# Performance work log

Hardware: AMD Instinct MI355X
Metric: run time of the kernel (lower is better)

Reference implementation:

```python
import jax, jax.numpy as jnp
import numpy as np

B, T, D, H = 512, 1024, 12, 100


def setup_inputs() -> dict:
    key = jax.random.key(0)
    ks = jax.random.split(key, 5)
    x = jax.random.normal(ks[0], (B, T, D), dtype=jnp.float32)
    Wx = jax.random.normal(ks[1], (D, 4 * H), dtype=jnp.float32) * (1.0 / np.sqrt(D))
    Wh = jax.random.normal(ks[2], (H, 4 * H), dtype=jnp.float32) * (1.0 / np.sqrt(H))
    b = jnp.zeros((4 * H,), dtype=jnp.float32)
    Wd = jax.random.normal(ks[3], (H, D), dtype=jnp.float32) * (1.0 / np.sqrt(H))
    bd = jnp.zeros((D,), dtype=jnp.float32)
    return {"x": x, "Wx": Wx, "Wh": Wh, "b": b, "Wd": Wd, "bd": bd}


def _lstm_seq(x, Wx, Wh, b):
    # Precompute input projection for all timesteps (vectorized GEMM).
    xg = jnp.einsum('btd,dh->bth', x, Wx) + b  # [B, T, 4H]
    xg = jnp.transpose(xg, (1, 0, 2))          # [T, B, 4H] for scan

    def step(carry, xg_t):
        h, c = carry
        z = xg_t + h @ Wh                      # [B, 4H]
        i, f, g, o = jnp.split(z, 4, axis=-1)  # Keras gate order: i, f, c, o
        i = jax.nn.sigmoid(i)
        f = jax.nn.sigmoid(f)
        g = jnp.tanh(g)
        o = jax.nn.sigmoid(o)
        c = f * c + i * g
        h = o * jnp.tanh(c)
        return (h, c), h

    h0 = jnp.zeros((x.shape[0], Wh.shape[0]), dtype=x.dtype)
    c0 = jnp.zeros_like(h0)
    _, hs = jax.lax.scan(step, (h0, c0), xg)   # hs: [T, B, H]
    return jnp.transpose(hs, (1, 0, 2))        # [B, T, H]


def reference(x, Wx, Wh, b, Wd, bd):
    hs = _lstm_seq(x, Wx, Wh, b)               # [B, T, H]
    return jnp.einsum('bth,hd->btd', hs, Wd) + bd  # [B, T, 12]
```

## Files before the change

kernel.cpp:

```cpp
#include <hip/hip_runtime.h>
#include <math.h>

#define T_LEN 1024
#define BATCH 512
#define DIN   12
#define HID   100
#define G4    400
#define MB    4
#define NBLK  (BATCH / MB)
#define AROW  160
#define NW    8
#define NTHR  (NW * 64)
#define CHUNK 64
#define UNROLL 8

typedef _Float16 half8   __attribute__((ext_vector_type(8)));
typedef _Float16 half4_t __attribute__((ext_vector_type(4)));
typedef float    f32x4   __attribute__((ext_vector_type(4)));

static __device__ __forceinline__ float fast_exp2(float v) {
#if __has_builtin(__builtin_amdgcn_exp2f)
    return __builtin_amdgcn_exp2f(v);
#else
    return exp2f(v);
#endif
}
static __device__ __forceinline__ float fast_rcp(float v) {
#if __has_builtin(__builtin_amdgcn_rcpf)
    return __builtin_amdgcn_rcpf(v);
#else
    return 1.0f / v;
#endif
}

static __device__ __forceinline__ void wg_barrier_lds() {
    __builtin_amdgcn_sched_barrier(0);
    asm volatile("s_waitcnt lgkmcnt(0)" ::: "memory");
    __builtin_amdgcn_s_barrier();
    __builtin_amdgcn_sched_barrier(0);
}

__launch_bounds__(NTHR, 2)
__global__ void lstm_mfma_kernel(const float* __restrict__ x,
                                 const float* __restrict__ Wx,
                                 const float* __restrict__ Wh,
                                 const float* __restrict__ b,
                                 const float* __restrict__ Wd,
                                 const float* __restrict__ bd,
                                 float* __restrict__ out) {
    __shared__ __align__(16) char smem[65536];
    const int tid  = threadIdx.x;
    const int wid  = tid >> 6;
    const int lane = tid & 63;
    const int l    = lane & 15;
    const int quad = lane >> 4;
    const int b0   = blockIdx.x * MB;
    const int j    = wid * 16 + l;

    const float L2E = 1.4426950408889634f;

    _Float16* stage = (_Float16*)smem;
    half8 bfrag[4][4];
#pragma unroll
    for (int pass = 0; pass < 2; ++pass) {
#pragma unroll
        for (int gg = 0; gg < 2; ++gg) {
            const int G = pass * 2 + gg;
            const float gsc = (G == 2) ? (-2.f * L2E) : (-L2E);
#pragma unroll
            for (int kt = 0; kt < 4; ++kt) {
                half8 v;
#pragma unroll
                for (int jj = 0; jj < 8; ++jj) {
                    const int k = kt * 32 + quad * 8 + jj;
                    float w = 0.f;
                    if (wid < 7) {
                        if (j < HID) {
                            if (k < HID)            w = Wh[k * G4 + G * HID + j] * gsc;
                            else if (k < HID + DIN) w = Wx[(k - HID) * G4 + G * HID + j] * gsc;
                        }
                    } else if (G == 0) {
                        if (l < DIN && k < HID)     w = Wd[k * DIN + l];
                    }
                    v[jj] = (_Float16)w;
                }
                *(half8*)&stage[((wid * 8) + (gg * 4 + kt)) * 512 + lane * 8] = v;
            }
        }
        __syncthreads();
#pragma unroll
        for (int gg = 0; gg < 2; ++gg)
#pragma unroll
            for (int kt = 0; kt < 4; ++kt)
                bfrag[pass * 2 + gg][kt] =
                    *(half8*)&stage[((wid * 8) + (gg * 4 + kt)) * 512 + lane * 8];
        __syncthreads();
    }

    f32x4 biasC[4];
#pragma unroll
    for (int G = 0; G < 4; ++G) biasC[G] = (f32x4){0.f, 0.f, 0.f, 0.f};
    if (wid < 7) {
        if (j < HID) {
#pragma unroll
            for (int G = 0; G < 4; ++G) {
                const float gsc = (G == 2) ? (-2.f * L2E) : (-L2E);
                const float bv = b[G * HID + j] * gsc;
                biasC[G] = (f32x4){bv, bv, bv, bv};
            }
        }
    } else if (l < DIN) {
        const float bv = bd[l];
        biasC[0] = (f32x4){bv, bv, bv, bv};
    }

    _Float16 (*Ah)[MB][AROW] = (_Float16 (*)[MB][AROW])smem;
    _Float16* xchunk = (_Float16*)(smem + 2560);

    auto refill = [&](int c) {
#pragma unroll
        for (int ii = 0; ii < 2; ++ii) {
            const int f = tid + NTHR * ii;
            if (f < (CHUNK * MB * DIN) / 4) {
                const int m  = f / (CHUNK * DIN / 4);
                const int o  = f - m * (CHUNK * DIN / 4);
                const int tt = o / 3;
                const int dd = o - tt * 3;
                const float4 v = *(const float4*)(x +
                    ((size_t)(b0 + m) * T_LEN + c * CHUNK + tt) * DIN + dd * 4);
                half4_t h4;
                h4[0] = (_Float16)v.x; h4[1] = (_Float16)v.y;
                h4[2] = (_Float16)v.z; h4[3] = (_Float16)v.w;
                *(half4_t*)&xchunk[tt * (MB * DIN) + m * DIN + dd * 4] = h4;
            }
        }
    };

    for (int i = tid; i < (2 * MB * AROW) / 2; i += NTHR) ((int*)smem)[i] = 0;
    refill(0);
    __syncthreads();
    if (tid < MB * 3) {
        const int m = tid / 3, part = tid - (tid / 3) * 3;
        *(half4_t*)&Ah[0][m][HID + part * 4] =
            *(const half4_t*)&xchunk[m * DIN + part * 4];
    }
    __syncthreads();

    const bool gate_lane = (wid < 7) && (j < HID);
    const int  arow = l >> 2;

    float cs = 0.f;
    float obuf[UNROLL];

#pragma unroll 1
    for (int tb = 0; tb < T_LEN / UNROLL; ++tb) {
#pragma unroll
        for (int it = 0; it < UNROLL; ++it) {
            const int t  = tb * UNROLL + it;
            const int p  = it & 1;
            const int pn = p ^ 1;

            if (it == UNROLL - 1) {
                if (((tb + 1) & 7) == 0 && (tb + 1) < T_LEN / UNROLL) {
                    refill((tb + 1) >> 3);
                    wg_barrier_lds();
                }
            }

            half8 a[4];
#pragma unroll
            for (int kt = 0; kt < 4; ++kt)
                a[kt] = *(const half8*)&Ah[p][arow][kt * 32 + quad * 8];

            if (wid < 7) {
                f32x4 acc[4];
#pragma unroll
                for (int kt = 0; kt < 4; ++kt)
#pragma unroll
                    for (int G = 0; G < 4; ++G)
                        acc[G] = __builtin_amdgcn_mfma_f32_16x16x32_f16(
                                     a[kt], bfrag[G][kt],
                                     (kt == 0) ? biasC[G] : acc[G], 0, 0, 0);

                if (gate_lane) {
                    const float ei = fast_exp2(acc[0][0]);
                    const float ef = fast_exp2(acc[1][0]);
                    const float eg = fast_exp2(acc[2][0]);
                    const float eo = fast_exp2(acc[3][0]);
                    const float gf  = fast_rcp(1.f + ef);
                    const float dd  = (1.f + ei) * (1.f + eg);
                    const float u   = __builtin_fmaf(eg, 2.f * L2E, -2.f * L2E);
                    const float gig = u * fast_rcp(dd);
                    cs = __builtin_fmaf(gf, cs, gig);
                    const float ec = fast_exp2(cs);
                    const float hv = (1.f - ec) * fast_rcp((1.f + eo) * (1.f + ec));
                    Ah[pn][quad][j] = (_Float16)hv;
                }
            } else {
                f32x4 accP;
#pragma unroll
                for (int kt = 0; kt < 4; ++kt)
                    accP = __builtin_amdgcn_mfma_f32_16x16x32_f16(
                               a[kt], bfrag[0][kt],
                               (kt == 0) ? biasC[0] : accP, 0, 0, 0);
                obuf[it] = accP[0];
                if ((t + 1) < T_LEN && lane < MB * 3) {
                    const int m = lane / 3, part = lane - (lane / 3) * 3;
                    *(half4_t*)&Ah[pn][m][HID + part * 4] =
                        *(const half4_t*)&xchunk[((t + 1) & (CHUNK - 1)) * (MB * DIN)
                                                 + m * DIN + part * 4];
                }
            }
            wg_barrier_lds();
        }
        if (wid == 7 && l < DIN) {
#pragma unroll
            for (int s = 0; s < UNROLL; ++s) {
                const int row = tb * UNROLL + s - 1;
                if (row >= 0)
                    out[((size_t)(b0 + quad) * T_LEN + row) * DIN + l] = obuf[s];
            }
        }
    }

    if (wid == 7) {
        half8 a[4];
#pragma unroll
        for (int kt = 0; kt < 4; ++kt)
            a[kt] = *(const half8*)&Ah[0][arow][kt * 32 + quad * 8];
        f32x4 accP;
#pragma unroll
        for (int kt = 0; kt < 4; ++kt)
            accP = __builtin_amdgcn_mfma_f32_16x16x32_f16(
                       a[kt], bfrag[0][kt],
                       (kt == 0) ? biasC[0] : accP, 0, 0, 0);
        if (l < DIN)
            out[((size_t)(b0 + quad) * T_LEN + (T_LEN - 1)) * DIN + l] = accP[0];
    }
}

extern "C" void kernel_launch(void* const* d_in, const int* in_sizes, int n_in,
                              void* d_out, int out_size, void* d_ws, size_t ws_size,
                              hipStream_t stream) {
    const float* x  = (const float*)d_in[0];
    const float* Wx = (const float*)d_in[1];
    const float* Wh = (const float*)d_in[2];
    const float* b  = (const float*)d_in[3];
    const float* Wd = (const float*)d_in[4];
    const float* bd = (const float*)d_in[5];
    float* out = (float*)d_out;

    lstm_mfma_kernel<<<NBLK, NTHR, 0, stream>>>(x, Wx, Wh, b, Wd, bd, out);
}
```

Before: 527.0 us.

## Process two independent batch groups per block to interleave recurrent chains

Each block now handles 8 batch rows as two independent groups of 4, with separate double-buffered hidden-state tiles, cell states and output buffers. Each step issues two sets of MFMAs and runs two gate computations, so the two dependency chains can overlap and the per-step barrier cost is spread over twice the work. The block count halves to 64, leaving fewer workgroups than CUs on the device. Register pressure and per-step latency also rise, and the refill loop now covers all 1536 float4 loads with no bounds guard.

```diff
diff --git a/kernel.cpp b/kernel.cpp
--- a/kernel.cpp
+++ b/kernel.cpp
@@ -6,7 +6,9 @@
 #define DIN   12
 #define HID   100
 #define G4    400
-#define MB    4
+#define MBG   4
+#define NG    2
+#define MB    (MBG * NG)
 #define NBLK  (BATCH / MB)
 #define AROW  160
 #define NW    8
@@ -114,34 +116,32 @@
         biasC[0] = (f32x4){bv, bv, bv, bv};
     }
 
-    _Float16 (*Ah)[MB][AROW] = (_Float16 (*)[MB][AROW])smem;
-    _Float16* xchunk = (_Float16*)(smem + 2560);
+    _Float16 (*Ah)[2][MBG][AROW] = (_Float16 (*)[2][MBG][AROW])smem;
+    _Float16* xchunk = (_Float16*)(smem + NG * 2 * MBG * AROW * 2);
 
     auto refill = [&](int c) {
 #pragma unroll
-        for (int ii = 0; ii < 2; ++ii) {
+        for (int ii = 0; ii < 3; ++ii) {
             const int f = tid + NTHR * ii;
-            if (f < (CHUNK * MB * DIN) / 4) {
-                const int m  = f / (CHUNK * DIN / 4);
-                const int o  = f - m * (CHUNK * DIN / 4);
-                const int tt = o / 3;
-                const int dd = o - tt * 3;
-                const float4 v = *(const float4*)(x +
-                    ((size_t)(b0 + m) * T_LEN + c * CHUNK + tt) * DIN + dd * 4);
-                half4_t h4;
-                h4[0] = (_Float16)v.x; h4[1] = (_Float16)v.y;
-                h4[2] = (_Float16)v.z; h4[3] = (_Float16)v.w;
-                *(half4_t*)&xchunk[tt * (MB * DIN) + m * DIN + dd * 4] = h4;
-            }
+            const int m  = f / (CHUNK * DIN / 4);
+            const int o  = f - m * (CHUNK * DIN / 4);
+            const int tt = o / 3;
+            const int dd = o - tt * 3;
+            const float4 v = *(const float4*)(x +
+                ((size_t)(b0 + m) * T_LEN + c * CHUNK + tt) * DIN + dd * 4);
+            half4_t h4;
+            h4[0] = (_Float16)v.x; h4[1] = (_Float16)v.y;
+            h4[2] = (_Float16)v.z; h4[3] = (_Float16)v.w;
+            *(half4_t*)&xchunk[tt * (MB * DIN) + m * DIN + dd * 4] = h4;
         }
     };
 
-    for (int i = tid; i < (2 * MB * AROW) / 2; i += NTHR) ((int*)smem)[i] = 0;
+    for (int i = tid; i < (NG * 2 * MBG * AROW) / 2; i += NTHR) ((int*)smem)[i] = 0;
     refill(0);
     __syncthreads();
     if (tid < MB * 3) {
         const int m = tid / 3, part = tid - (tid / 3) * 3;
-        *(half4_t*)&Ah[0][m][HID + part * 4] =
+        *(half4_t*)&Ah[m >> 2][0][m & 3][HID + part * 4] =
             *(const half4_t*)&xchunk[m * DIN + part * 4];
     }
     __syncthreads();
@@ -149,8 +149,22 @@
     const bool gate_lane = (wid < 7) && (j < HID);
     const int  arow = l >> 2;
 
-    float cs = 0.f;
-    float obuf[UNROLL];
+    float csA = 0.f, csB = 0.f;
+    float obufA[UNROLL], obufB[UNROLL];
+
+    auto cell = [&](const f32x4* acc, float& cs_) -> float {
+        const float ei = fast_exp2(acc[0][0]);
+        const float ef = fast_exp2(acc[1][0]);
+        const float eg = fast_exp2(acc[2][0]);
+        const float eo = fast_exp2(acc[3][0]);
+        const float gf  = fast_rcp(1.f + ef);
+        const float dd  = (1.f + ei) * (1.f + eg);
+        const float u   = __builtin_fmaf(eg, 2.f * L2E, -2.f * L2E);
+        const float gig = u * fast_rcp(dd);
+        cs_ = __builtin_fmaf(gf, cs_, gig);
+        const float ec = fast_exp2(cs_);
+        return (1.f - ec) * fast_rcp((1.f + eo) * (1.f + ec));
+    };
 
 #pragma unroll 1
     for (int tb = 0; tb < T_LEN / UNROLL; ++tb) {
@@ -167,46 +181,54 @@
                 }
             }
 
-            half8 a[4];
+            half8 aA[4], aB[4];
 #pragma unroll
             for (int kt = 0; kt < 4; ++kt)
-                a[kt] = *(const half8*)&Ah[p][arow][kt * 32 + quad * 8];
+                aA[kt] = *(const half8*)&Ah[0][p][arow][kt * 32 + quad * 8];
+#pragma unroll
+            for (int kt = 0; kt < 4; ++kt)
+                aB[kt] = *(const half8*)&Ah[1][p][arow][kt * 32 + quad * 8];
 
             if (wid < 7) {
-                f32x4 acc[4];
+                f32x4 accA[4], accB[4];
 #pragma unroll
                 for (int kt = 0; kt < 4; ++kt)
 #pragma unroll
                     for (int G = 0; G < 4; ++G)
-                        acc[G] = __builtin_amdgcn_mfma_f32_16x16x32_f16(
-                                     a[kt], bfrag[G][kt],
-                                     (kt == 0) ? biasC[G] : acc[G], 0, 0, 0);
+                        accA[G] = __builtin_amdgcn_mfma_f32_16x16x32_f16(
+                                      aA[kt], bfrag[G][kt],
+                                      (kt == 0) ? biasC[G] : accA[G], 0, 0, 0);
+#pragma unroll
+                for (int kt = 0; kt < 4; ++kt)
+#pragma unroll
+                    for (int G = 0; G < 4; ++G)
+                        accB[G] = __builtin_amdgcn_mfma_f32_16x16x32_f16(
+                                      aB[kt], bfrag[G][kt],
+                                      (kt == 0) ? biasC[G] : accB[G], 0, 0, 0);
 
                 if (gate_lane) {
-                    const float ei = fast_exp2(acc[0][0]);
-                    const float ef = fast_exp2(acc[1][0]);
-                    const float eg = fast_exp2(acc[2][0]);
-                    const float eo = fast_exp2(acc[3][0]);
-                    const float gf  = fast_rcp(1.f + ef);
-                    const float dd  = (1.f + ei) * (1.f + eg);
-                    const float u   = __builtin_fmaf(eg, 2.f * L2E, -2.f * L2E);
-                    const float gig = u * fast_rcp(dd);
-                    cs = __builtin_fmaf(gf, cs, gig);
-                    const float ec = fast_exp2(cs);
-                    const float hv = (1.f - ec) * fast_rcp((1.f + eo) * (1.f + ec));
-                    Ah[pn][quad][j] = (_Float16)hv;
+                    const float hA = cell(accA, csA);
+                    const float hB = cell(accB, csB);
+                    Ah[0][pn][quad][j] = (_Float16)hA;
+                    Ah[1][pn][quad][j] = (_Float16)hB;
                 }
             } else {
-                f32x4 accP;
-#pragma unroll
-                for (int kt = 0; kt < 4; ++kt)
-                    accP = __builtin_amdgcn_mfma_f32_16x16x32_f16(
-                               a[kt], bfrag[0][kt],
-                               (kt == 0) ? biasC[0] : accP, 0, 0, 0);
-                obuf[it] = accP[0];
+                f32x4 accPA, accPB;
+#pragma unroll
+                for (int kt = 0; kt < 4; ++kt)
+                    accPA = __builtin_amdgcn_mfma_f32_16x16x32_f16(
+                                aA[kt], bfrag[0][kt],
+                                (kt == 0) ? biasC[0] : accPA, 0, 0, 0);
+#pragma unroll
+                for (int kt = 0; kt < 4; ++kt)
+                    accPB = __builtin_amdgcn_mfma_f32_16x16x32_f16(
+                                aB[kt], bfrag[0][kt],
+                                (kt == 0) ? biasC[0] : accPB, 0, 0, 0);
+                obufA[it] = accPA[0];
+                obufB[it] = accPB[0];
                 if ((t + 1) < T_LEN && lane < MB * 3) {
                     const int m = lane / 3, part = lane - (lane / 3) * 3;
-                    *(half4_t*)&Ah[pn][m][HID + part * 4] =
+                    *(half4_t*)&Ah[m >> 2][pn][m & 3][HID + part * 4] =
                         *(const half4_t*)&xchunk[((t + 1) & (CHUNK - 1)) * (MB * DIN)
                                                  + m * DIN + part * 4];
                 }
@@ -217,25 +239,36 @@
 #pragma unroll
             for (int s = 0; s < UNROLL; ++s) {
                 const int row = tb * UNROLL + s - 1;
-                if (row >= 0)
-                    out[((size_t)(b0 + quad) * T_LEN + row) * DIN + l] = obuf[s];
+                if (row >= 0) {
+                    out[((size_t)(b0 + quad) * T_LEN + row) * DIN + l] = obufA[s];
+                    out[((size_t)(b0 + MBG + quad) * T_LEN + row) * DIN + l] = obufB[s];
+                }
             }
         }
     }
 
     if (wid == 7) {
-        half8 a[4];
+        half8 aA[4], aB[4];
+#pragma unroll
+        for (int kt = 0; kt < 4; ++kt) {
+            aA[kt] = *(const half8*)&Ah[0][0][arow][kt * 32 + quad * 8];
+            aB[kt] = *(const half8*)&Ah[1][0][arow][kt * 32 + quad * 8];
+        }
+        f32x4 accPA, accPB;
 #pragma unroll
         for (int kt = 0; kt < 4; ++kt)
-            a[kt] = *(const half8*)&Ah[0][arow][kt * 32 + quad * 8];
-        f32x4 accP;
+            accPA = __builtin_amdgcn_mfma_f32_16x16x32_f16(
+                        aA[kt], bfrag[0][kt],
+                        (kt == 0) ? biasC[0] : accPA, 0, 0, 0);
 #pragma unroll
         for (int kt = 0; kt < 4; ++kt)
-            accP = __builtin_amdgcn_mfma_f32_16x16x32_f16(
-                       a[kt], bfrag[0][kt],
-                       (kt == 0) ? biasC[0] : accP, 0, 0, 0);
-        if (l < DIN)
-            out[((size_t)(b0 + quad) * T_LEN + (T_LEN - 1)) * DIN + l] = accP[0];
+            accPB = __builtin_amdgcn_mfma_f32_16x16x32_f16(
+                        aB[kt], bfrag[0][kt],
+                        (kt == 0) ? biasC[0] : accPB, 0, 0, 0);
+        if (l < DIN) {
+            out[((size_t)(b0 + quad) * T_LEN + (T_LEN - 1)) * DIN + l] = accPA[0];
+            out[((size_t)(b0 + MBG + quad) * T_LEN + (T_LEN - 1)) * DIN + l] = accPB[0];
+        }
     }
 }
 
```

Result: slower. 857.3 us (+62.7%).

## Halve waves per block, give each wave two hidden-unit tiles

Applied to the files above, without the earlier changes.

Reduces the workgroup from 8 to 4 waves. Each of waves 0-2 now computes two 16-column gate tiles, and wave 3 computes one gate tile plus the output projection. The goal is a cheaper per-timestep workgroup barrier and fewer idle lanes in the serial recurrence. In exchange each wave issues more MFMAs and cell math per step, which lengthens the critical path, and register pressure rises since twice the B fragments are held.

```diff
diff --git a/kernel.cpp b/kernel.cpp
--- a/kernel.cpp
+++ b/kernel.cpp
@@ -9,7 +9,7 @@
 #define MB    4
 #define NBLK  (BATCH / MB)
 #define AROW  160
-#define NW    8
+#define NW    4
 #define NTHR  (NW * 64)
 #define CHUNK 64
 #define UNROLL 8
@@ -40,7 +40,7 @@
     __builtin_amdgcn_sched_barrier(0);
 }
 
-__launch_bounds__(NTHR, 2)
+__launch_bounds__(NTHR, 1)
 __global__ void lstm_mfma_kernel(const float* __restrict__ x,
                                  const float* __restrict__ Wx,
                                  const float* __restrict__ Wh,
@@ -48,24 +48,24 @@
                                  const float* __restrict__ Wd,
                                  const float* __restrict__ bd,
                                  float* __restrict__ out) {
-    __shared__ __align__(16) char smem[65536];
+    __shared__ __align__(16) char smem[32768];
     const int tid  = threadIdx.x;
     const int wid  = tid >> 6;
     const int lane = tid & 63;
     const int l    = lane & 15;
     const int quad = lane >> 4;
     const int b0   = blockIdx.x * MB;
-    const int j    = wid * 16 + l;
 
     const float L2E = 1.4426950408889634f;
 
     _Float16* stage = (_Float16*)smem;
-    half8 bfrag[4][4];
-#pragma unroll
-    for (int pass = 0; pass < 2; ++pass) {
+    half8 bfrag[2][4][4];
+#pragma unroll
+    for (int pass = 0; pass < 4; ++pass) {
+        const int ti = pass >> 1;
 #pragma unroll
         for (int gg = 0; gg < 2; ++gg) {
-            const int G = pass * 2 + gg;
+            const int G = (pass & 1) * 2 + gg;
             const float gsc = (G == 2) ? (-2.f * L2E) : (-L2E);
 #pragma unroll
             for (int kt = 0; kt < 4; ++kt) {
@@ -74,10 +74,12 @@
                 for (int jj = 0; jj < 8; ++jj) {
                     const int k = kt * 32 + quad * 8 + jj;
                     float w = 0.f;
-                    if (wid < 7) {
-                        if (j < HID) {
-                            if (k < HID)            w = Wh[k * G4 + G * HID + j] * gsc;
-                            else if (k < HID + DIN) w = Wx[(k - HID) * G4 + G * HID + j] * gsc;
+                    if (!(wid == 3 && ti == 1)) {
+                        const int tt = (ti == 0) ? wid : wid + 4;
+                        const int jc = tt * 16 + l;
+                        if (jc < HID) {
+                            if (k < HID)            w = Wh[k * G4 + G * HID + jc] * gsc;
+                            else if (k < HID + DIN) w = Wx[(k - HID) * G4 + G * HID + jc] * gsc;
                         }
                     } else if (G == 0) {
                         if (l < DIN && k < HID)     w = Wd[k * DIN + l];
@@ -92,26 +94,38 @@
         for (int gg = 0; gg < 2; ++gg)
 #pragma unroll
             for (int kt = 0; kt < 4; ++kt)
-                bfrag[pass * 2 + gg][kt] =
+                bfrag[ti][(pass & 1) * 2 + gg][kt] =
                     *(half8*)&stage[((wid * 8) + (gg * 4 + kt)) * 512 + lane * 8];
         __syncthreads();
     }
 
-    f32x4 biasC[4];
-#pragma unroll
-    for (int G = 0; G < 4; ++G) biasC[G] = (f32x4){0.f, 0.f, 0.f, 0.f};
-    if (wid < 7) {
-        if (j < HID) {
-#pragma unroll
-            for (int G = 0; G < 4; ++G) {
-                const float gsc = (G == 2) ? (-2.f * L2E) : (-L2E);
-                const float bv = b[G * HID + j] * gsc;
-                biasC[G] = (f32x4){bv, bv, bv, bv};
-            }
-        }
-    } else if (l < DIN) {
-        const float bv = bd[l];
-        biasC[0] = (f32x4){bv, bv, bv, bv};
+    f32x4 biasC[2][4];
+#pragma unroll
+    for (int ti = 0; ti < 2; ++ti)
+#pragma unroll
+        for (int G = 0; G < 4; ++G) biasC[ti][G] = (f32x4){0.f, 0.f, 0.f, 0.f};
+    {
+        const int jc0 = wid * 16 + l;
+#pragma unroll
+        for (int G = 0; G < 4; ++G) {
+            const float gsc = (G == 2) ? (-2.f * L2E) : (-L2E);
+            const float bv = b[G * HID + jc0] * gsc;
+            biasC[0][G] = (f32x4){bv, bv, bv, bv};
+        }
+        if (wid < 3) {
+            const int jc1 = (wid + 4) * 16 + l;
+            if (jc1 < HID) {
+#pragma unroll
+                for (int G = 0; G < 4; ++G) {
+                    const float gsc = (G == 2) ? (-2.f * L2E) : (-L2E);
+                    const float bv = b[G * HID + jc1] * gsc;
+                    biasC[1][G] = (f32x4){bv, bv, bv, bv};
+                }
+            }
+        } else if (l < DIN) {
+            const float bv = bd[l];
+            biasC[1][0] = (f32x4){bv, bv, bv, bv};
+        }
     }
 
     _Float16 (*Ah)[MB][AROW] = (_Float16 (*)[MB][AROW])smem;
@@ -119,20 +133,18 @@
 
     auto refill = [&](int c) {
 #pragma unroll
-        for (int ii = 0; ii < 2; ++ii) {
+        for (int ii = 0; ii < 3; ++ii) {
             const int f = tid + NTHR * ii;
-            if (f < (CHUNK * MB * DIN) / 4) {
-                const int m  = f / (CHUNK * DIN / 4);
-                const int o  = f - m * (CHUNK * DIN / 4);
-                const int tt = o / 3;
-                const int dd = o - tt * 3;
-                const float4 v = *(const float4*)(x +
-                    ((size_t)(b0 + m) * T_LEN + c * CHUNK + tt) * DIN + dd * 4);
-                half4_t h4;
-                h4[0] = (_Float16)v.x; h4[1] = (_Float16)v.y;
-                h4[2] = (_Float16)v.z; h4[3] = (_Float16)v.w;
-                *(half4_t*)&xchunk[tt * (MB * DIN) + m * DIN + dd * 4] = h4;
-            }
+            const int m  = f / (CHUNK * DIN / 4);
+            const int o  = f - m * (CHUNK * DIN / 4);
+            const int tt = o / 3;
+            const int dd = o - tt * 3;
+            const float4 v = *(const float4*)(x +
+                ((size_t)(b0 + m) * T_LEN + c * CHUNK + tt) * DIN + dd * 4);
+            half4_t h4;
+            h4[0] = (_Float16)v.x; h4[1] = (_Float16)v.y;
+            h4[2] = (_Float16)v.z; h4[3] = (_Float16)v.w;
+            *(half4_t*)&xchunk[tt * (MB * DIN) + m * DIN + dd * 4] = h4;
         }
     };
 
@@ -146,11 +158,24 @@
     }
     __syncthreads();
 
-    const bool gate_lane = (wid < 7) && (j < HID);
-    const int  arow = l >> 2;
-
-    float cs = 0.f;
+    const int arow = l >> 2;
+
+    float csA = 0.f, csB = 0.f;
     float obuf[UNROLL];
+
+    auto cell = [&](const f32x4* acc, float& cs_) -> float {
+        const float ei = fast_exp2(acc[0][0]);
+        const float ef = fast_exp2(acc[1][0]);
+        const float eg = fast_exp2(acc[2][0]);
+        const float eo = fast_exp2(acc[3][0]);
+        const float gf  = fast_rcp(1.f + ef);
+        const float dd  = (1.f + ei) * (1.f + eg);
+        const float u   = __builtin_fmaf(eg, 2.f * L2E, -2.f * L2E);
+        const float gig = u * fast_rcp(dd);
+        cs_ = __builtin_fmaf(gf, cs_, gig);
+        const float ec = fast_exp2(cs_);
+        return (1.f - ec) * fast_rcp((1.f + eo) * (1.f + ec));
+    };
 
 #pragma unroll 1
     for (int tb = 0; tb < T_LEN / UNROLL; ++tb) {
@@ -172,37 +197,38 @@
             for (int kt = 0; kt < 4; ++kt)
                 a[kt] = *(const half8*)&Ah[p][arow][kt * 32 + quad * 8];
 
-            if (wid < 7) {
-                f32x4 acc[4];
+            if (wid < 3) {
+                f32x4 acc[2][4];
 #pragma unroll
                 for (int kt = 0; kt < 4; ++kt)
 #pragma unroll
+                    for (int ti = 0; ti < 2; ++ti)
+#pragma unroll
+                        for (int G = 0; G < 4; ++G)
+                            acc[ti][G] = __builtin_amdgcn_mfma_f32_16x16x32_f16(
+                                             a[kt], bfrag[ti][G][kt],
+                                             (kt == 0) ? biasC[ti][G] : acc[ti][G], 0, 0, 0);
+
+                const float hA = cell(acc[0], csA);
+                const float hB = cell(acc[1], csB);
+                Ah[pn][quad][wid * 16 + l] = (_Float16)hA;
+                if (wid < 2 || l < 4)
+                    Ah[pn][quad][(wid + 4) * 16 + l] = (_Float16)hB;
+            } else {
+                f32x4 acc3[4], accP;
+#pragma unroll
+                for (int kt = 0; kt < 4; ++kt) {
+#pragma unroll
                     for (int G = 0; G < 4; ++G)
-                        acc[G] = __builtin_amdgcn_mfma_f32_16x16x32_f16(
-                                     a[kt], bfrag[G][kt],
-                                     (kt == 0) ? biasC[G] : acc[G], 0, 0, 0);
-
-                if (gate_lane) {
-                    const float ei = fast_exp2(acc[0][0]);
-                    const float ef = fast_exp2(acc[1][0]);
-                    const float eg = fast_exp2(acc[2][0]);
-                    const float eo = fast_exp2(acc[3][0]);
-                    const float gf  = fast_rcp(1.f + ef);
-                    const float dd  = (1.f + ei) * (1.f + eg);
-                    const float u   = __builtin_fmaf(eg, 2.f * L2E, -2.f * L2E);
-                    const float gig = u * fast_rcp(dd);
-                    cs = __builtin_fmaf(gf, cs, gig);
-                    const float ec = fast_exp2(cs);
-                    const float hv = (1.f - ec) * fast_rcp((1.f + eo) * (1.f + ec));
-                    Ah[pn][quad][j] = (_Float16)hv;
-                }
-            } else {
-                f32x4 accP;
-#pragma unroll
-                for (int kt = 0; kt < 4; ++kt)
+                        acc3[G] = __builtin_amdgcn_mfma_f32_16x16x32_f16(
+                                      a[kt], bfrag[0][G][kt],
+                                      (kt == 0) ? biasC[0][G] : acc3[G], 0, 0, 0);
                     accP = __builtin_amdgcn_mfma_f32_16x16x32_f16(
-                               a[kt], bfrag[0][kt],
-                               (kt == 0) ? biasC[0] : accP, 0, 0, 0);
+                               a[kt], bfrag[1][0][kt],
+                               (kt == 0) ? biasC[1][0] : accP, 0, 0, 0);
+                }
+                const float h3 = cell(acc3, csA);
+                Ah[pn][quad][48 + l] = (_Float16)h3;
                 obuf[it] = accP[0];
                 if ((t + 1) < T_LEN && lane < MB * 3) {
                     const int m = lane / 3, part = lane - (lane / 3) * 3;
@@ -213,7 +239,7 @@
             }
             wg_barrier_lds();
         }
-        if (wid == 7 && l < DIN) {
+        if (wid == 3 && l < DIN) {
 #pragma unroll
             for (int s = 0; s < UNROLL; ++s) {
                 const int row = tb * UNROLL + s - 1;
@@ -223,7 +249,7 @@
         }
     }
 
-    if (wid == 7) {
+    if (wid == 3) {
         half8 a[4];
 #pragma unroll
         for (int kt = 0; kt < 4; ++kt)
@@ -232,8 +258,8 @@
 #pragma unroll
         for (int kt = 0; kt < 4; ++kt)
             accP = __builtin_amdgcn_mfma_f32_16x16x32_f16(
-                       a[kt], bfrag[0][kt],
-                       (kt == 0) ? biasC[0] : accP, 0, 0, 0);
+                       a[kt], bfrag[1][0][kt],
+                       (kt == 0) ? biasC[1][0] : accP, 0, 0, 0);
         if (l < DIN)
             out[((size_t)(b0 + quad) * T_LEN + (T_LEN - 1)) * DIN + l] = accP[0];
     }
```

Result: slower. 642.7 us (+22.0%).
